# Performance work log

Hardware: AMD Instinct MI355X
Metric: run time of the kernel (lower is better)

Reference implementation:

```python
import jax, jax.numpy as jnp
import numpy as np

B, N, M = 4, 2048, 2048
QUERY_DIM = 512
CONTEXT_DIM = 512
HEADS = 8
DIM_HEAD = 64
INNER = HEADS * DIM_HEAD  # 512
SCALE = DIM_HEAD ** -0.5


def setup_inputs() -> dict:
    key = jax.random.key(0)
    ks = jax.random.split(key, 7)
    x = jax.random.normal(ks[0], (B, N, QUERY_DIM), dtype=jnp.float32)
    context = jax.random.normal(ks[1], (B, M, CONTEXT_DIM), dtype=jnp.float32)
    mask = jax.random.randint(ks[2], (B, M), 0, 2) > 0  # bool key mask
    # Kaiming-uniform-ish init scale, like nn.Linear defaults
    Wq = jax.random.uniform(ks[3], (QUERY_DIM, INNER), dtype=jnp.float32,
                            minval=-1, maxval=1) * (QUERY_DIM ** -0.5)
    Wkv = jax.random.uniform(ks[4], (CONTEXT_DIM, 2 * INNER), dtype=jnp.float32,
                             minval=-1, maxval=1) * (CONTEXT_DIM ** -0.5)
    Wo = jax.random.uniform(ks[5], (INNER, QUERY_DIM), dtype=jnp.float32,
                            minval=-1, maxval=1) * (INNER ** -0.5)
    bo = jax.random.uniform(ks[6], (QUERY_DIM,), dtype=jnp.float32,
                            minval=-1, maxval=1) * (INNER ** -0.5)
    return {"x": x, "context": context, "mask": mask,
            "Wq": Wq, "Wkv": Wkv, "Wo": Wo, "bo": bo}


def reference(x, context, mask, Wq, Wkv, Wo, bo):
    # projections (no bias for q/kv, bias for out — as in the torch module)
    q = x @ Wq                       # [b, n, inner]
    kv = context @ Wkv               # [b, m, 2*inner]
    k, v = jnp.split(kv, 2, axis=-1)
    # split heads: b n (h d) -> b h n d
    def split_heads(t):
        b, n, _ = t.shape
        return t.reshape(b, n, HEADS, DIM_HEAD).transpose(0, 2, 1, 3)
    q, k, v = split_heads(q), split_heads(k), split_heads(v)
    sim = jnp.einsum('bhid,bhjd->bhij', q, k) * SCALE  # [b, h, n, m]
    max_neg = -jnp.finfo(sim.dtype).max
    sim = jnp.where(mask[:, None, None, :], sim, max_neg)
    attn = jax.nn.softmax(sim, axis=-1)
    out = jnp.einsum('bhij,bhjd->bhid', attn, v)       # [b, h, n, d]
    out = out.transpose(0, 2, 1, 3).reshape(x.shape[0], x.shape[1], INNER)
    return out @ Wo + bo
```

## Files before the change

kernel.cpp:

```cpp
#include <hip/hip_runtime.h>
#include <hip/hip_bf16.h>
#include <cstddef>

typedef __attribute__((ext_vector_type(8))) short short8;
typedef __attribute__((ext_vector_type(4))) float f32x4;

__device__ inline unsigned short f2bf(float f) {
  unsigned int u = __float_as_uint(f);
  u += 0x7fffu + ((u >> 16) & 1u);
  return (unsigned short)(u >> 16);
}
__device__ inline unsigned int pkbf(float a, float b) {
  __hip_bfloat162 h = __float22bfloat162_rn(make_float2(a, b));
  union { __hip_bfloat162 h2; unsigned int u; } cv;
  cv.h2 = h;
  return cv.u;
}
__device__ inline float bf2f_lo(unsigned int u) {
  return __uint_as_float(u << 16);
}
__device__ inline float bf2f_hi(unsigned int u) {
  return __uint_as_float(u & 0xFFFF0000u);
}

__global__ __launch_bounds__(256) void prep_kernel(
    const float* __restrict__ Wq, const float* __restrict__ Wkv,
    const float* __restrict__ Wo, const int* __restrict__ mask,
    unsigned short* __restrict__ Wq_t, unsigned short* __restrict__ Wkv_t,
    unsigned short* __restrict__ Wo_t, unsigned int* __restrict__ pmask) {
  const int z = blockIdx.z;
  if (z == 3) {
    if (blockIdx.y != 0) return;
    int idx = blockIdx.x * 256 + threadIdx.x;
    int bb = idx >> 10, rem = idx & 1023;
    int g = rem >> 5, rem2 = rem & 31;
    int lqv = rem2 >> 3, e = rem2 & 7;
    int ct = e >> 1, half = e & 1;
    int key0 = g * 64 + half * 32 + lqv * 8 + 2 * ct;
    const int* mb = mask + bb * 2048;
    pmask[idx] = (mb[key0] ? 0xFFFFu : 0u) | (mb[key0 + 1] ? 0xFFFF0000u : 0u);
    return;
  }
  const float* src = (z == 0) ? Wq : (z == 1) ? Wkv : Wo;
  unsigned short* dst = (z == 0) ? Wq_t : (z == 1) ? Wkv_t : Wo_t;
  const int R = 512, C = (z == 1) ? 1024 : 512;
  if (blockIdx.x * 64 >= C) return;
  __shared__ float tile[64][65];
  int c0 = blockIdx.x * 64, r0 = blockIdx.y * 64;
  int tx = threadIdx.x & 63, ty = threadIdx.x >> 6;
  for (int i = ty; i < 64; i += 4)
    tile[i][tx] = src[(size_t)(r0 + i) * C + c0 + tx];
  __syncthreads();
  for (int i = ty; i < 64; i += 4)
    dst[(size_t)(c0 + i) * R + r0 + tx] = f2bf(tile[tx][i]);
}

__global__ __launch_bounds__(256, 3) void proj_kernel(
    const float* __restrict__ x, const float* __restrict__ context,
    const unsigned short* __restrict__ Wq_t, const unsigned short* __restrict__ Wkv_t,
    unsigned short* __restrict__ qb, unsigned short* __restrict__ kb,
    unsigned short* __restrict__ vtb, float qscale) {
  __shared__ unsigned short As[128][72];
  __shared__ unsigned short Bs[128][72];
  const int bid = blockIdx.x;
  const bool isq = bid < 256;
  const int lid = isq ? bid : bid - 256;
  const float* Af = isq ? x : context;
  const unsigned short* Bt = isq ? Wq_t : Wkv_t;
  const int bn = (isq ? (lid & 3) : (lid & 7)) * 128;
  const int bm = (isq ? (lid >> 2) : (lid >> 3)) * 128;
  const int K = 512;
  const int tid = threadIdx.x;
  const int wave = tid >> 6, lane = tid & 63;
  const int wr = (wave >> 1) * 64, wc = (wave & 1) * 64;
  const int l15 = lane & 15, lq = lane >> 4;
  const int sr = tid >> 3, sc = (tid & 7) * 8;
  f32x4 acc[4][4] = {};

  float4 fA0a = *(const float4*)(Af + (size_t)(bm + sr) * K + sc);
  float4 fA0b = *(const float4*)(Af + (size_t)(bm + sr) * K + sc + 4);
  float4 fA1a = *(const float4*)(Af + (size_t)(bm + sr + 32) * K + sc);
  float4 fA1b = *(const float4*)(Af + (size_t)(bm + sr + 32) * K + sc + 4);
  float4 fA2a = *(const float4*)(Af + (size_t)(bm + sr + 64) * K + sc);
  float4 fA2b = *(const float4*)(Af + (size_t)(bm + sr + 64) * K + sc + 4);
  float4 fA3a = *(const float4*)(Af + (size_t)(bm + sr + 96) * K + sc);
  float4 fA3b = *(const float4*)(Af + (size_t)(bm + sr + 96) * K + sc + 4);
  uint4 uB0 = *(const uint4*)(Bt + (size_t)(bn + sr) * K + sc);
  uint4 uB1 = *(const uint4*)(Bt + (size_t)(bn + sr + 32) * K + sc);
  uint4 uB2 = *(const uint4*)(Bt + (size_t)(bn + sr + 64) * K + sc);
  uint4 uB3 = *(const uint4*)(Bt + (size_t)(bn + sr + 96) * K + sc);

  for (int k0 = 0; k0 < K; k0 += 64) {
    __syncthreads();
    uint4 u;
    u.x = pkbf(fA0a.x, fA0a.y); u.y = pkbf(fA0a.z, fA0a.w);
    u.z = pkbf(fA0b.x, fA0b.y); u.w = pkbf(fA0b.z, fA0b.w);
    *(uint4*)(&As[sr][sc]) = u;
    u.x = pkbf(fA1a.x, fA1a.y); u.y = pkbf(fA1a.z, fA1a.w);
    u.z = pkbf(fA1b.x, fA1b.y); u.w = pkbf(fA1b.z, fA1b.w);
    *(uint4*)(&As[sr + 32][sc]) = u;
    u.x = pkbf(fA2a.x, fA2a.y); u.y = pkbf(fA2a.z, fA2a.w);
    u.z = pkbf(fA2b.x, fA2b.y); u.w = pkbf(fA2b.z, fA2b.w);
    *(uint4*)(&As[sr + 64][sc]) = u;
    u.x = pkbf(fA3a.x, fA3a.y); u.y = pkbf(fA3a.z, fA3a.w);
    u.z = pkbf(fA3b.x, fA3b.y); u.w = pkbf(fA3b.z, fA3b.w);
    *(uint4*)(&As[sr + 96][sc]) = u;
    *(uint4*)(&Bs[sr][sc])      = uB0;
    *(uint4*)(&Bs[sr + 32][sc]) = uB1;
    *(uint4*)(&Bs[sr + 64][sc]) = uB2;
    *(uint4*)(&Bs[sr + 96][sc]) = uB3;
    __syncthreads();
    if (k0 + 64 < K) {
      const int kn = k0 + 64;
      fA0a = *(const float4*)(Af + (size_t)(bm + sr) * K + kn + sc);
      fA0b = *(const float4*)(Af + (size_t)(bm + sr) * K + kn + sc + 4);
      fA1a = *(const float4*)(Af + (size_t)(bm + sr + 32) * K + kn + sc);
      fA1b = *(const float4*)(Af + (size_t)(bm + sr + 32) * K + kn + sc + 4);
      fA2a = *(const float4*)(Af + (size_t)(bm + sr + 64) * K + kn + sc);
      fA2b = *(const float4*)(Af + (size_t)(bm + sr + 64) * K + kn + sc + 4);
      fA3a = *(const float4*)(Af + (size_t)(bm + sr + 96) * K + kn + sc);
      fA3b = *(const float4*)(Af + (size_t)(bm + sr + 96) * K + kn + sc + 4);
      uB0 = *(const uint4*)(Bt + (size_t)(bn + sr) * K + kn + sc);
      uB1 = *(const uint4*)(Bt + (size_t)(bn + sr + 32) * K + kn + sc);
      uB2 = *(const uint4*)(Bt + (size_t)(bn + sr + 64) * K + kn + sc);
      uB3 = *(const uint4*)(Bt + (size_t)(bn + sr + 96) * K + kn + sc);
    }
#pragma unroll
    for (int kk = 0; kk < 2; ++kk) {
      short8 af[4], bfr[4];
#pragma unroll
      for (int mt = 0; mt < 4; ++mt)
        af[mt] = *(const short8*)(&As[wr + mt * 16 + l15][kk * 32 + lq * 8]);
#pragma unroll
      for (int nt = 0; nt < 4; ++nt)
        bfr[nt] = *(const short8*)(&Bs[wc + nt * 16 + l15][kk * 32 + lq * 8]);
#pragma unroll
      for (int mt = 0; mt < 4; ++mt)
#pragma unroll
        for (int nt = 0; nt < 4; ++nt)
          acc[mt][nt] = __builtin_amdgcn_mfma_f32_16x16x32_bf16(af[mt], bfr[nt], acc[mt][nt], 0, 0, 0);
    }
  }

#pragma unroll
  for (int mt = 0; mt < 4; ++mt)
#pragma unroll
    for (int nt = 0; nt < 4; ++nt) {
      int row0 = bm + wr + mt * 16 + lq * 4;
      int col = bn + wc + nt * 16 + l15;
      if (isq) {
#pragma unroll
        for (int j = 0; j < 4; ++j)
          qb[(size_t)(row0 + j) * 512 + col] = f2bf(acc[mt][nt][j] * qscale);
      } else if (col < 512) {
#pragma unroll
        for (int j = 0; j < 4; ++j)
          kb[(size_t)(row0 + j) * 512 + col] = f2bf(acc[mt][nt][j]);
      } else {
        int bb = row0 >> 11, m = row0 & 2047;
        int hd = col - 512;
        uint2 w;
        w.x = pkbf(acc[mt][nt][0], acc[mt][nt][1]);
        w.y = pkbf(acc[mt][nt][2], acc[mt][nt][3]);
        *(uint2*)(vtb + ((size_t)bb * 512 + hd) * 2048 + m) = w;
      }
    }
}

__global__ __launch_bounds__(256) void outproj_kernel(
    const unsigned short* __restrict__ poA, const unsigned short* __restrict__ poB,
    const float* __restrict__ ls, const unsigned short* __restrict__ Bt,
    float* __restrict__ C0, const float* __restrict__ bias) {
  __shared__ unsigned short As[64][72];
  __shared__ unsigned short Bs[128][72];
  __shared__ float rls[512];
  const int bm = blockIdx.y * 64, bn = blockIdx.x * 128;
  const int K = 512, N = 512;
  const int tid = threadIdx.x;
  const int wave = tid >> 6, lane = tid & 63;
  const int wr = (wave >> 1) * 32, wc = (wave & 1) * 64;
  const int l15 = lane & 15, lq = lane >> 4;
  const int sr = tid >> 3, sc = (tid & 7) * 8;
  f32x4 acc[2][4] = {};

#pragma unroll
  for (int it = 0; it < 2; ++it) {
    int idx = tid + it * 256;
    int hh = idx >> 6, row = bm + (idx & 63);
    rls[idx] = 1.0f / (ls[(size_t)hh * 8192 + row] + ls[65536 + (size_t)hh * 8192 + row]);
  }

  for (int k0 = 0; k0 < K; k0 += 64) {
    const int h = k0 >> 6;
    __syncthreads();
#pragma unroll
    for (int p = 0; p < 2; ++p) {
      int row = bm + sr + p * 32;
      uint4 ua = *(const uint4*)(poA + (size_t)row * 512 + k0 + sc);
      uint4 ub = *(const uint4*)(poB + (size_t)row * 512 + k0 + sc);
      float rl = rls[h * 64 + sr + p * 32];
      uint4 u;
      u.x = pkbf((bf2f_lo(ua.x) + bf2f_lo(ub.x)) * rl, (bf2f_hi(ua.x) + bf2f_hi(ub.x)) * rl);
      u.y = pkbf((bf2f_lo(ua.y) + bf2f_lo(ub.y)) * rl, (bf2f_hi(ua.y) + bf2f_hi(ub.y)) * rl);
      u.z = pkbf((bf2f_lo(ua.z) + bf2f_lo(ub.z)) * rl, (bf2f_hi(ua.z) + bf2f_hi(ub.z)) * rl);
      u.w = pkbf((bf2f_lo(ua.w) + bf2f_lo(ub.w)) * rl, (bf2f_hi(ua.w) + bf2f_hi(ub.w)) * rl);
      *(uint4*)(&As[sr + p * 32][sc]) = u;
    }
#pragma unroll
    for (int p = 0; p < 4; ++p)
      *(uint4*)(&Bs[sr + p * 32][sc]) = *(const uint4*)(Bt + (size_t)(bn + sr + p * 32) * K + k0 + sc);
    __syncthreads();
#pragma unroll
    for (int kk = 0; kk < 2; ++kk) {
      short8 af[2], bfr[4];
#pragma unroll
      for (int mt = 0; mt < 2; ++mt)
        af[mt] = *(const short8*)(&As[wr + mt * 16 + l15][kk * 32 + lq * 8]);
#pragma unroll
      for (int nt = 0; nt < 4; ++nt)
        bfr[nt] = *(const short8*)(&Bs[wc + nt * 16 + l15][kk * 32 + lq * 8]);
#pragma unroll
      for (int mt = 0; mt < 2; ++mt)
#pragma unroll
        for (int nt = 0; nt < 4; ++nt)
          acc[mt][nt] = __builtin_amdgcn_mfma_f32_16x16x32_bf16(af[mt], bfr[nt], acc[mt][nt], 0, 0, 0);
    }
  }

#pragma unroll
  for (int mt = 0; mt < 2; ++mt)
#pragma unroll
    for (int nt = 0; nt < 4; ++nt) {
      int row0 = bm + wr + mt * 16 + lq * 4;
      int col = bn + wc + nt * 16 + l15;
#pragma unroll
      for (int j = 0; j < 4; ++j)
        C0[(size_t)(row0 + j) * N + col] = acc[mt][nt][j] + bias[col];
    }
}

__global__ __launch_bounds__(256, 3) void attn_kernel(
    const unsigned short* __restrict__ Q, const unsigned short* __restrict__ Kb,
    const unsigned short* __restrict__ Vt, const unsigned int* __restrict__ pmask,
    unsigned short* __restrict__ poA, unsigned short* __restrict__ poB,
    float* __restrict__ ls) {
  __shared__ unsigned short Ks[2][64][72];
  __shared__ unsigned short Vs[2][64][72];
  const int b = blockIdx.x >> 3, h = blockIdx.x & 7;
  const int z = blockIdx.z;
  const int tid = threadIdx.x, lane = tid & 63;
  const int wave = tid >> 6;
  const int l15 = lane & 15, lq = lane >> 4;
  const int wrow = blockIdx.y * 128 + wave * 32;

  const unsigned short* Qr0 = Q + (size_t)(b * 2048 + wrow + l15) * 512 + h * 64;
  const unsigned short* Qr1 = Q + (size_t)(b * 2048 + wrow + 16 + l15) * 512 + h * 64;
  short8 q00 = *(const short8*)(Qr0 + lq * 8);
  short8 q01 = *(const short8*)(Qr0 + 32 + lq * 8);
  short8 q10 = *(const short8*)(Qr1 + lq * 8);
  short8 q11 = *(const short8*)(Qr1 + 32 + lq * 8);

  const short8 vones = {0x3F80, 0x3F80, 0x3F80, 0x3F80,
                        0x3F80, 0x3F80, 0x3F80, 0x3F80};

  f32x4 o0[4] = {}, o1[4] = {};
  f32x4 ol0 = {}, ol1 = {};

  const unsigned short* Kg = Kb + (size_t)b * 2048 * 512 + h * 64;
  const unsigned short* Vg = Vt + (size_t)(b * 8 + h) * 64 * 2048;
  const unsigned int* Pm = pmask + b * 1024;

  const int str = tid >> 3;
  const int stc = (tid & 7) * 8;
  const int kprow = ((str & 7) >> 1) * 16 + ((str >> 3) & 3) * 4 + (str & 1);

  const int mb0 = z << 10;

  uint4 krA0 = *(const uint4*)(Kg + (size_t)(mb0 + str) * 512 + stc);
  uint4 krA1 = *(const uint4*)(Kg + (size_t)(mb0 + str + 32) * 512 + stc);
  uint4 krB0 = *(const uint4*)(Kg + (size_t)(mb0 + 64 + str) * 512 + stc);
  uint4 krB1 = *(const uint4*)(Kg + (size_t)(mb0 + 64 + str + 32) * 512 + stc);
  uint4 vrA0 = *(const uint4*)(Vg + (size_t)str * 2048 + mb0 + stc);
  uint4 vrA1 = *(const uint4*)(Vg + (size_t)(str + 32) * 2048 + mb0 + stc);
  uint4 vrB0 = *(const uint4*)(Vg + (size_t)str * 2048 + mb0 + 64 + stc);
  uint4 vrB1 = *(const uint4*)(Vg + (size_t)(str + 32) * 2048 + mb0 + 64 + stc);

  for (int mb = mb0; mb < mb0 + 1024; mb += 128) {
    __syncthreads();
    *(uint4*)(&Ks[0][kprow][stc])     = krA0;
    *(uint4*)(&Ks[0][kprow + 2][stc]) = krA1;
    *(uint4*)(&Ks[1][kprow][stc])     = krB0;
    *(uint4*)(&Ks[1][kprow + 2][stc]) = krB1;
    *(uint4*)(&Vs[0][str][stc])       = vrA0;
    *(uint4*)(&Vs[0][str + 32][stc])  = vrA1;
    *(uint4*)(&Vs[1][str][stc])       = vrB0;
    *(uint4*)(&Vs[1][str + 32][stc])  = vrB1;
    __syncthreads();
    if (mb + 128 < mb0 + 1024) {
      const int nx = mb + 128;
      krA0 = *(const uint4*)(Kg + (size_t)(nx + str) * 512 + stc);
      krA1 = *(const uint4*)(Kg + (size_t)(nx + str + 32) * 512 + stc);
      krB0 = *(const uint4*)(Kg + (size_t)(nx + 64 + str) * 512 + stc);
      krB1 = *(const uint4*)(Kg + (size_t)(nx + 64 + str + 32) * 512 + stc);
      vrA0 = *(const uint4*)(Vg + (size_t)str * 2048 + nx + stc);
      vrA1 = *(const uint4*)(Vg + (size_t)(str + 32) * 2048 + nx + stc);
      vrB0 = *(const uint4*)(Vg + (size_t)str * 2048 + nx + 64 + stc);
      vrB1 = *(const uint4*)(Vg + (size_t)(str + 32) * 2048 + nx + 64 + stc);
    }

#pragma unroll
    for (int g = 0; g < 2; ++g) {
      const uint4 m0 = *(const uint4*)(Pm + ((mb >> 6) + g) * 32 + lq * 8);
      const uint4 m1 = *(const uint4*)(Pm + ((mb >> 6) + g) * 32 + lq * 8 + 4);

      f32x4 s0[4] = {}, s1[4] = {};
#pragma unroll
      for (int ct = 0; ct < 4; ++ct) {
        short8 kf = *(const short8*)(&Ks[g][ct * 16 + l15][lq * 8]);
        s0[ct] = __builtin_amdgcn_mfma_f32_16x16x32_bf16(kf, q00, s0[ct], 0, 0, 0);
        s1[ct] = __builtin_amdgcn_mfma_f32_16x16x32_bf16(kf, q10, s1[ct], 0, 0, 0);
      }
#pragma unroll
      for (int ct = 0; ct < 4; ++ct) {
        short8 kf = *(const short8*)(&Ks[g][ct * 16 + l15][32 + lq * 8]);
        s0[ct] = __builtin_amdgcn_mfma_f32_16x16x32_bf16(kf, q01, s0[ct], 0, 0, 0);
        s1[ct] = __builtin_amdgcn_mfma_f32_16x16x32_bf16(kf, q11, s1[ct], 0, 0, 0);
      }

      unsigned int xp0[4][2], xp1[4][2];
#pragma unroll
      for (int ct = 0; ct < 4; ++ct) {
        float a0 = __builtin_amdgcn_exp2f(s0[ct][0]);
        float a1 = __builtin_amdgcn_exp2f(s0[ct][1]);
        float a2 = __builtin_amdgcn_exp2f(s0[ct][2]);
        float a3 = __builtin_amdgcn_exp2f(s0[ct][3]);
        xp0[ct][0] = pkbf(a0, a1);
        xp0[ct][1] = pkbf(a2, a3);
        float c0 = __builtin_amdgcn_exp2f(s1[ct][0]);
        float c1 = __builtin_amdgcn_exp2f(s1[ct][1]);
        float c2 = __builtin_amdgcn_exp2f(s1[ct][2]);
        float c3 = __builtin_amdgcn_exp2f(s1[ct][3]);
        xp1[ct][0] = pkbf(c0, c1);
        xp1[ct][1] = pkbf(c2, c3);
      }

      xp0[0][0] &= m0.x; xp0[0][1] &= m0.y; xp0[1][0] &= m0.z; xp0[1][1] &= m0.w;
      xp0[2][0] &= m1.x; xp0[2][1] &= m1.y; xp0[3][0] &= m1.z; xp0[3][1] &= m1.w;
      xp1[0][0] &= m0.x; xp1[0][1] &= m0.y; xp1[1][0] &= m0.z; xp1[1][1] &= m0.w;
      xp1[2][0] &= m1.x; xp1[2][1] &= m1.y; xp1[3][0] &= m1.z; xp1[3][1] &= m1.w;

#pragma unroll
      for (int kk = 0; kk < 2; ++kk) {
        union { unsigned int u[4]; short8 s8; } pc0, pc1;
        pc0.u[0] = xp0[0][kk]; pc0.u[1] = xp0[1][kk];
        pc0.u[2] = xp0[2][kk]; pc0.u[3] = xp0[3][kk];
        pc1.u[0] = xp1[0][kk]; pc1.u[1] = xp1[1][kk];
        pc1.u[2] = xp1[2][kk]; pc1.u[3] = xp1[3][kk];
#pragma unroll
        for (int dt = 0; dt < 4; ++dt) {
          short8 vf = *(const short8*)(&Vs[g][dt * 16 + l15][kk * 32 + lq * 8]);
          o0[dt] = __builtin_amdgcn_mfma_f32_16x16x32_bf16(vf, pc0.s8, o0[dt], 0, 0, 0);
          o1[dt] = __builtin_amdgcn_mfma_f32_16x16x32_bf16(vf, pc1.s8, o1[dt], 0, 0, 0);
        }
        ol0 = __builtin_amdgcn_mfma_f32_16x16x32_bf16(vones, pc0.s8, ol0, 0, 0, 0);
        ol1 = __builtin_amdgcn_mfma_f32_16x16x32_bf16(vones, pc1.s8, ol1, 0, 0, 0);
      }
    }
  }

  unsigned short* po = z ? poB : poA;
  unsigned short* Or0 = po + (size_t)(b * 2048 + wrow + l15) * 512 + h * 64;
  unsigned short* Or1 = po + (size_t)(b * 2048 + wrow + 16 + l15) * 512 + h * 64;
#pragma unroll
  for (int dt = 0; dt < 4; ++dt) {
    *(unsigned int*)(Or0 + dt * 16 + lq * 4)     = pkbf(o0[dt][0], o0[dt][1]);
    *(unsigned int*)(Or0 + dt * 16 + lq * 4 + 2) = pkbf(o0[dt][2], o0[dt][3]);
    *(unsigned int*)(Or1 + dt * 16 + lq * 4)     = pkbf(o1[dt][0], o1[dt][1]);
    *(unsigned int*)(Or1 + dt * 16 + lq * 4 + 2) = pkbf(o1[dt][2], o1[dt][3]);
  }
  if (lq == 0) {
    ls[((size_t)z * 8 + h) * 8192 + b * 2048 + wrow + l15]      = ol0[0];
    ls[((size_t)z * 8 + h) * 8192 + b * 2048 + wrow + 16 + l15] = ol1[0];
  }
}

extern "C" void kernel_launch(void* const* d_in, const int* in_sizes, int n_in,
                              void* d_out, int out_size, void* d_ws, size_t ws_size,
                              hipStream_t stream) {
  const float* x       = (const float*)d_in[0];
  const float* context = (const float*)d_in[1];
  const int*   mask    = (const int*)d_in[2];
  const float* Wq      = (const float*)d_in[3];
  const float* Wkv     = (const float*)d_in[4];
  const float* Wo      = (const float*)d_in[5];
  const float* bo      = (const float*)d_in[6];
  float* out = (float*)d_out;

  char* ws = (char*)d_ws;
  unsigned short* Wq_t  = (unsigned short*)(ws + 0);
  unsigned short* Wkv_t = (unsigned short*)(ws + 524288);
  unsigned short* Wo_t  = (unsigned short*)(ws + 1572864);
  unsigned short* qb    = (unsigned short*)(ws + 2097152);
  unsigned short* kb    = (unsigned short*)(ws + 10485760);
  unsigned short* vtb   = (unsigned short*)(ws + 18874368);
  unsigned short* poA   = (unsigned short*)(ws + 27262976);
  unsigned short* poB   = (unsigned short*)(ws + 35651584);
  unsigned int* pmask   = (unsigned int*)(ws + 44040192);
  float* ls             = (float*)(ws + 44056576);

  const float QSCALE = 0.125f * 1.44269504088896f;

  prep_kernel<<<dim3(16, 8, 4), 256, 0, stream>>>(Wq, Wkv, Wo, mask,
                                                  Wq_t, Wkv_t, Wo_t, pmask);
  proj_kernel<<<dim3(768), 256, 0, stream>>>(x, context, Wq_t, Wkv_t,
                                             qb, kb, vtb, QSCALE);
  attn_kernel<<<dim3(32, 16, 2), 256, 0, stream>>>(qb, kb, vtb, pmask,
                                                   poA, poB, ls);
  outproj_kernel<<<dim3(4, 128), 256, 0, stream>>>(poA, poB, ls, Wo_t, out, bo);
}
```

Measured before the change: 104.3 us.

## Drop register prefetch of K/V tiles and raise attention occupancy to 4 blocks

Removes the register-staged software prefetch of the next K and V tiles in the attention kernel and loads global memory straight into shared memory each iteration. It also raises the launch-bounds minimum from 3 to 4 blocks per CU. Freeing the 32 prefetch registers per thread should let more waves stay resident so that other blocks hide latency. In exchange, each iteration now waits on its global loads before computing, with no overlap inside a block.

```diff
diff --git a/kernel.cpp b/kernel.cpp
--- a/kernel.cpp
+++ b/kernel.cpp
@@ -239,7 +239,7 @@
     }
 }
 
-__global__ __launch_bounds__(256, 3) void attn_kernel(
+__global__ __launch_bounds__(256, 4) void attn_kernel(
     const unsigned short* __restrict__ Q, const unsigned short* __restrict__ Kb,
     const unsigned short* __restrict__ Vt, const unsigned int* __restrict__ pmask,
     unsigned short* __restrict__ poA, unsigned short* __restrict__ poB,
@@ -276,37 +276,17 @@
 
   const int mb0 = z << 10;
 
-  uint4 krA0 = *(const uint4*)(Kg + (size_t)(mb0 + str) * 512 + stc);
-  uint4 krA1 = *(const uint4*)(Kg + (size_t)(mb0 + str + 32) * 512 + stc);
-  uint4 krB0 = *(const uint4*)(Kg + (size_t)(mb0 + 64 + str) * 512 + stc);
-  uint4 krB1 = *(const uint4*)(Kg + (size_t)(mb0 + 64 + str + 32) * 512 + stc);
-  uint4 vrA0 = *(const uint4*)(Vg + (size_t)str * 2048 + mb0 + stc);
-  uint4 vrA1 = *(const uint4*)(Vg + (size_t)(str + 32) * 2048 + mb0 + stc);
-  uint4 vrB0 = *(const uint4*)(Vg + (size_t)str * 2048 + mb0 + 64 + stc);
-  uint4 vrB1 = *(const uint4*)(Vg + (size_t)(str + 32) * 2048 + mb0 + 64 + stc);
-
   for (int mb = mb0; mb < mb0 + 1024; mb += 128) {
     __syncthreads();
-    *(uint4*)(&Ks[0][kprow][stc])     = krA0;
-    *(uint4*)(&Ks[0][kprow + 2][stc]) = krA1;
-    *(uint4*)(&Ks[1][kprow][stc])     = krB0;
-    *(uint4*)(&Ks[1][kprow + 2][stc]) = krB1;
-    *(uint4*)(&Vs[0][str][stc])       = vrA0;
-    *(uint4*)(&Vs[0][str + 32][stc])  = vrA1;
-    *(uint4*)(&Vs[1][str][stc])       = vrB0;
-    *(uint4*)(&Vs[1][str + 32][stc])  = vrB1;
-    __syncthreads();
-    if (mb + 128 < mb0 + 1024) {
-      const int nx = mb + 128;
-      krA0 = *(const uint4*)(Kg + (size_t)(nx + str) * 512 + stc);
-      krA1 = *(const uint4*)(Kg + (size_t)(nx + str + 32) * 512 + stc);
-      krB0 = *(const uint4*)(Kg + (size_t)(nx + 64 + str) * 512 + stc);
-      krB1 = *(const uint4*)(Kg + (size_t)(nx + 64 + str + 32) * 512 + stc);
-      vrA0 = *(const uint4*)(Vg + (size_t)str * 2048 + nx + stc);
-      vrA1 = *(const uint4*)(Vg + (size_t)(str + 32) * 2048 + nx + stc);
-      vrB0 = *(const uint4*)(Vg + (size_t)str * 2048 + nx + 64 + stc);
-      vrB1 = *(const uint4*)(Vg + (size_t)(str + 32) * 2048 + nx + 64 + stc);
-    }
+    *(uint4*)(&Ks[0][kprow][stc])     = *(const uint4*)(Kg + (size_t)(mb + str) * 512 + stc);
+    *(uint4*)(&Ks[0][kprow + 2][stc]) = *(const uint4*)(Kg + (size_t)(mb + str + 32) * 512 + stc);
+    *(uint4*)(&Ks[1][kprow][stc])     = *(const uint4*)(Kg + (size_t)(mb + 64 + str) * 512 + stc);
+    *(uint4*)(&Ks[1][kprow + 2][stc]) = *(const uint4*)(Kg + (size_t)(mb + 64 + str + 32) * 512 + stc);
+    *(uint4*)(&Vs[0][str][stc])       = *(const uint4*)(Vg + (size_t)str * 2048 + mb + stc);
+    *(uint4*)(&Vs[0][str + 32][stc])  = *(const uint4*)(Vg + (size_t)(str + 32) * 2048 + mb + stc);
+    *(uint4*)(&Vs[1][str][stc])       = *(const uint4*)(Vg + (size_t)str * 2048 + mb + 64 + stc);
+    *(uint4*)(&Vs[1][str + 32][stc])  = *(const uint4*)(Vg + (size_t)(str + 32) * 2048 + mb + 64 + stc);
+    __syncthreads();
 
 #pragma unroll
     for (int g = 0; g < 2; ++g) {
```

New measurement: 110.7 us. +6.2%, slower.
